# Kernel tuning notes

Measured on AMD Instinct MI355X. Metric: run time of the kernel, lower is better.

The kernel has to match this reference:

```python
import jax, jax.numpy as jnp
import numpy as np

DIM = 384

def setup_inputs() -> dict:
    key = jax.random.key(0)
    k1, k2, k3 = jax.random.split(key, 3)
    x = jax.random.normal(k1, (8, DIM, 56, 56), dtype=jnp.float32)
    # nn.Linear(dim, dim, bias=False): weight shape [out, in]; y = x @ W^T
    w1 = jax.random.normal(k2, (DIM, DIM), dtype=jnp.float32) * (1.0 / np.sqrt(DIM))
    w2 = jax.random.normal(k3, (DIM, DIM), dtype=jnp.float32) * (1.0 / np.sqrt(DIM))
    return {"x": x, "w1": w1, "w2": w2}

def reference(x, w1, w2):
    B, C, H, W = x.shape
    scale = C ** (-0.5)
    t = x.reshape(B, C, H * W).transpose(0, 2, 1)  # [B, N, C]
    q = jnp.einsum('bnc,dc->bnd', t, w1)           # linear1(x)
    attn = jnp.einsum('bnd,bmd->bnm', q, t) * scale  # QK^T scaled
    attn = jax.nn.softmax(attn, axis=-1)
    v = jnp.einsum('bnc,dc->bnd', t, w2)           # linear2(x)
    out = jnp.einsum('bnm,bmd->bnd', attn, v)      # [B, N, C]
    return out.transpose(0, 2, 1).reshape(B, C, H, W)
```

## Files before the change

### kernel.cpp

```cpp
#include <hip/hip_runtime.h>
#include <hip/hip_bf16.h>

#define DIM 384
#define SEQ 3136
#define NBATCH 8

typedef __attribute__((ext_vector_type(8))) short short8;
typedef __attribute__((ext_vector_type(4))) float fx4;
typedef __attribute__((ext_vector_type(4))) int i4;
typedef __hip_bfloat16 bf16;

#define MFMA(a,b,c) __builtin_amdgcn_mfma_f32_16x16x32_bf16(a,b,c,0,0,0)

__global__ __launch_bounds__(256) void ktrans(const float* __restrict__ x,
                                              bf16* __restrict__ kb) {
  __shared__ float t[64][65];
  int b = blockIdx.z;
  int n0 = blockIdx.x * 64, c0 = blockIdx.y * 64;
  int tid = threadIdx.x;
  {
    int nl = tid & 63, cl = tid >> 6;
    const float* xp = x + ((size_t)b * DIM + c0) * SEQ + n0;
    #pragma unroll
    for (int p = 0; p < 16; ++p) {
      int c = cl * 16 + p;
      t[c][nl] = xp[(size_t)c * SEQ + nl];
    }
  }
  __syncthreads();
  {
    int cc = tid & 63, nr = tid >> 6;
    bf16* kp = kb + ((size_t)b * SEQ + n0) * DIM + c0;
    #pragma unroll
    for (int p = 0; p < 16; ++p) {
      int n = nr * 16 + p;
      kp[(size_t)n * DIM + cc] = __float2bfloat16(t[cc][n]);
    }
  }
}

__global__ __launch_bounds__(256) void kwconv(const float* __restrict__ w1,
                                              const float* __restrict__ w2,
                                              bf16* __restrict__ w1b,
                                              bf16* __restrict__ w2b) {
  int i = blockIdx.x * 256 + threadIdx.x;
  w1b[i] = __float2bfloat16(w1[i]);
  w2b[i] = __float2bfloat16(w2[i]);
}

__global__ __launch_bounds__(256, 1) void kgemm(const bf16* __restrict__ A, long long Abs,
                                                const bf16* __restrict__ Bt, long long Bbs,
                                                bf16* __restrict__ out, long long Obs, int ldo) {
  __shared__ __align__(16) bf16 At[64][DIM + 8];
  __shared__ __align__(16) bf16 Bs[64][DIM + 8];
  int b = blockIdx.z;
  int tid = threadIdx.x;
  const bf16* Ab = A + (size_t)b * Abs + (size_t)blockIdx.x * 64 * DIM;
  const bf16* Bb = Bt + (size_t)b * Bbs + (size_t)blockIdx.y * 64 * DIM;
  {
    int row = tid >> 2, cb = (tid & 3) * 96;
    const i4* ga = (const i4*)(Ab + (size_t)row * DIM + cb);
    const i4* gb = (const i4*)(Bb + (size_t)row * DIM + cb);
    i4* la = (i4*)(&At[row][cb]);
    i4* lb = (i4*)(&Bs[row][cb]);
    #pragma unroll
    for (int p = 0; p < 12; ++p) { la[p] = ga[p]; lb[p] = gb[p]; }
  }
  __syncthreads();
  int wave = tid >> 6, lane = tid & 63;
  int r = lane & 15, kq = lane >> 4;
  fx4 zero = {0.f, 0.f, 0.f, 0.f};
  fx4 acc[4];
  #pragma unroll
  for (int i = 0; i < 4; ++i) acc[i] = zero;
  #pragma unroll
  for (int ks = 0; ks < 12; ++ks) {
    short8 af = *(const short8*)(&At[wave * 16 + r][ks * 32 + kq * 8]);
    #pragma unroll
    for (int ct = 0; ct < 4; ++ct) {
      short8 bfr = *(const short8*)(&Bs[ct * 16 + r][ks * 32 + kq * 8]);
      acc[ct] = MFMA(af, bfr, acc[ct]);
    }
  }
  bf16* ob = out + (size_t)b * Obs
           + (size_t)(blockIdx.x * 64 + wave * 16 + kq * 4) * ldo + blockIdx.y * 64;
  #pragma unroll
  for (int ct = 0; ct < 4; ++ct)
    #pragma unroll
    for (int rr = 0; rr < 4; ++rr)
      ob[(size_t)rr * ldo + ct * 16 + r] = __float2bfloat16(acc[ct][rr]);
}

__global__ __launch_bounds__(256, 2) void kattn(const bf16* __restrict__ Qb,
                                                const bf16* __restrict__ Kb,
                                                const bf16* __restrict__ Vt,
                                                float* __restrict__ out) {
  __shared__ __align__(16) bf16 Kl[64][DIM + 8];
  __shared__ __align__(16) bf16 Pl[4][16][68];
  __shared__ float rsum[64];

  int b = blockIdx.x;
  int n0 = blockIdx.y * 64;
  int tid = threadIdx.x;
  int wave = tid >> 6, lane = tid & 63;
  int r = lane & 15, kq = lane >> 4;

  short8 qf[12];
  {
    const bf16* qp = Qb + ((size_t)b * SEQ + n0 + wave * 16 + r) * DIM + kq * 8;
    #pragma unroll
    for (int ks = 0; ks < 12; ++ks) qf[ks] = *(const short8*)(qp + ks * 32);
  }
  fx4 zero = {0.f, 0.f, 0.f, 0.f};
  fx4 acc[4][6];
  #pragma unroll
  for (int i = 0; i < 4; ++i)
    #pragma unroll
    for (int j = 0; j < 6; ++j) acc[i][j] = zero;
  float rs[4] = {0.f, 0.f, 0.f, 0.f};
  const float cexp = 0.07362223f;

  const bf16* kbase = Kb + (size_t)b * SEQ * DIM;
  const bf16* vbase = Vt + (size_t)b * DIM * SEQ;

  int srow = tid >> 2, scb = (tid & 3) * 96;

  for (int im = 0; im < SEQ / 64; ++im) {
    int m0 = im * 64;
    {
      const i4* g = (const i4*)(kbase + (size_t)(m0 + srow) * DIM + scb);
      i4* l = (i4*)(&Kl[srow][scb]);
      #pragma unroll
      for (int p = 0; p < 12; ++p) l[p] = g[p];
    }
    short8 vf[2][6];
    #pragma unroll
    for (int ks2 = 0; ks2 < 2; ++ks2)
      #pragma unroll
      for (int dtl = 0; dtl < 6; ++dtl) {
        int d = (wave * 6 + dtl) * 16 + r;
        vf[ks2][dtl] = *(const short8*)(vbase + (size_t)d * SEQ + m0 + ks2 * 32 + kq * 8);
      }
    __syncthreads();
    fx4 sa[4];
    #pragma unroll
    for (int ct = 0; ct < 4; ++ct) sa[ct] = zero;
    #pragma unroll
    for (int ks = 0; ks < 12; ++ks) {
      #pragma unroll
      for (int ct = 0; ct < 4; ++ct) {
        short8 bfr = *(const short8*)(&Kl[ct * 16 + r][ks * 32 + kq * 8]);
        sa[ct] = MFMA(qf[ks], bfr, sa[ct]);
      }
    }
    #pragma unroll
    for (int rr = 0; rr < 4; ++rr) {
      float e0 = exp2f(sa[0][rr] * cexp);
      float e1 = exp2f(sa[1][rr] * cexp);
      float e2 = exp2f(sa[2][rr] * cexp);
      float e3 = exp2f(sa[3][rr] * cexp);
      int row = kq * 4 + rr;
      Pl[wave][row][r]      = __float2bfloat16(e0);
      Pl[wave][row][16 + r] = __float2bfloat16(e1);
      Pl[wave][row][32 + r] = __float2bfloat16(e2);
      Pl[wave][row][48 + r] = __float2bfloat16(e3);
      rs[rr] += (e0 + e1) + (e2 + e3);
    }
    __syncthreads();
    #pragma unroll
    for (int ks2 = 0; ks2 < 2; ++ks2) {
      short8 pa[4];
      #pragma unroll
      for (int rg = 0; rg < 4; ++rg)
        pa[rg] = *(const short8*)(&Pl[rg][r][ks2 * 32 + kq * 8]);
      #pragma unroll
      for (int dtl = 0; dtl < 6; ++dtl) {
        #pragma unroll
        for (int rg = 0; rg < 4; ++rg)
          acc[rg][dtl] = MFMA(pa[rg], vf[ks2][dtl], acc[rg][dtl]);
      }
    }
  }
  #pragma unroll
  for (int rr = 0; rr < 4; ++rr) {
    float v = rs[rr];
    v += __shfl_xor(v, 1);
    v += __shfl_xor(v, 2);
    v += __shfl_xor(v, 4);
    v += __shfl_xor(v, 8);
    if (r == 0) rsum[wave * 16 + kq * 4 + rr] = v;
  }
  __syncthreads();
  float* ob = out + (size_t)b * DIM * SEQ;
  #pragma unroll
  for (int rg = 0; rg < 4; ++rg) {
    #pragma unroll
    for (int rr = 0; rr < 4; ++rr) {
      float inv = 1.0f / rsum[rg * 16 + kq * 4 + rr];
      int n = n0 + rg * 16 + kq * 4 + rr;
      #pragma unroll
      for (int dtl = 0; dtl < 6; ++dtl) {
        int d = (wave * 6 + dtl) * 16 + r;
        ob[(size_t)d * SEQ + n] = acc[rg][dtl][rr] * inv;
      }
    }
  }
}

extern "C" void kernel_launch(void* const* d_in, const int* in_sizes, int n_in,
                              void* d_out, int out_size, void* d_ws, size_t ws_size,
                              hipStream_t stream) {
  const float* x  = (const float*)d_in[0];
  const float* w1 = (const float*)d_in[1];
  const float* w2 = (const float*)d_in[2];
  float* out = (float*)d_out;

  char* ws = (char*)d_ws;
  size_t SZ = (size_t)NBATCH * SEQ * DIM * sizeof(bf16);
  bf16* Kb  = (bf16*)(ws);
  bf16* Qb  = (bf16*)(ws + SZ);
  bf16* Vt  = (bf16*)(ws + 2 * SZ);
  bf16* w1b = (bf16*)(ws + 3 * SZ);
  bf16* w2b = (bf16*)(ws + 3 * SZ + (size_t)DIM * DIM * sizeof(bf16));

  ktrans<<<dim3(SEQ / 64, DIM / 64, NBATCH), 256, 0, stream>>>(x, Kb);
  kwconv<<<dim3(DIM * DIM / 256), 256, 0, stream>>>(w1, w2, w1b, w2b);
  kgemm<<<dim3(SEQ / 64, DIM / 64, NBATCH), 256, 0, stream>>>(
      Kb, (long long)SEQ * DIM, w1b, 0LL, Qb, (long long)SEQ * DIM, DIM);
  kgemm<<<dim3(DIM / 64, SEQ / 64, NBATCH), 256, 0, stream>>>(
      w2b, 0LL, Kb, (long long)SEQ * DIM, Vt, (long long)DIM * SEQ, SEQ);
  kattn<<<dim3(NBATCH, SEQ / 64), 256, 0, stream>>>(Qb, Kb, Vt, out);
}
```

Measured before the change: 305.7 us.

## Repartition attention kernel to 32-row query tiles with 8 waves per block

The attention kernel now processes 32 query rows per block with 512 threads. Waves split into 2 row groups times 4 key-column chunks for the QK^T stage, and each wave owns 48 output channels for the PV stage. Per-wave row sums are combined through shared memory. This doubles the block count and cuts per-thread accumulator registers, aiming for more occupancy and better latency hiding. In exchange, each K tile is loaded from global and LDS-staged twice as often per query row, which raises K/V traffic.

```diff
diff --git a/kernel.cpp b/kernel.cpp
--- a/kernel.cpp
+++ b/kernel.cpp
@@ -91,93 +91,83 @@
       ob[(size_t)rr * ldo + ct * 16 + r] = __float2bfloat16(acc[ct][rr]);
 }
 
-__global__ __launch_bounds__(256, 2) void kattn(const bf16* __restrict__ Qb,
+__global__ __launch_bounds__(512, 4) void kattn(const bf16* __restrict__ Qb,
                                                 const bf16* __restrict__ Kb,
                                                 const bf16* __restrict__ Vt,
                                                 float* __restrict__ out) {
   __shared__ __align__(16) bf16 Kl[64][DIM + 8];
-  __shared__ __align__(16) bf16 Pl[4][16][68];
-  __shared__ float rsum[64];
+  __shared__ __align__(16) bf16 Pl[2][16][68];
+  __shared__ float rsum2[4][32];
 
   int b = blockIdx.x;
-  int n0 = blockIdx.y * 64;
+  int n0 = blockIdx.y * 32;
   int tid = threadIdx.x;
   int wave = tid >> 6, lane = tid & 63;
   int r = lane & 15, kq = lane >> 4;
+  int rg = wave >> 2;
+  int ch = wave & 3;
 
   short8 qf[12];
   {
-    const bf16* qp = Qb + ((size_t)b * SEQ + n0 + wave * 16 + r) * DIM + kq * 8;
+    const bf16* qp = Qb + ((size_t)b * SEQ + n0 + rg * 16 + r) * DIM + kq * 8;
     #pragma unroll
     for (int ks = 0; ks < 12; ++ks) qf[ks] = *(const short8*)(qp + ks * 32);
   }
   fx4 zero = {0.f, 0.f, 0.f, 0.f};
-  fx4 acc[4][6];
-  #pragma unroll
-  for (int i = 0; i < 4; ++i)
-    #pragma unroll
-    for (int j = 0; j < 6; ++j) acc[i][j] = zero;
+  fx4 acc[2][3];
+  #pragma unroll
+  for (int i = 0; i < 2; ++i)
+    #pragma unroll
+    for (int j = 0; j < 3; ++j) acc[i][j] = zero;
   float rs[4] = {0.f, 0.f, 0.f, 0.f};
   const float cexp = 0.07362223f;
 
   const bf16* kbase = Kb + (size_t)b * SEQ * DIM;
   const bf16* vbase = Vt + (size_t)b * DIM * SEQ;
 
-  int srow = tid >> 2, scb = (tid & 3) * 96;
+  int krow = tid >> 3, kcs = (tid & 7) * 48;
 
   for (int im = 0; im < SEQ / 64; ++im) {
     int m0 = im * 64;
     {
-      const i4* g = (const i4*)(kbase + (size_t)(m0 + srow) * DIM + scb);
-      i4* l = (i4*)(&Kl[srow][scb]);
-      #pragma unroll
-      for (int p = 0; p < 12; ++p) l[p] = g[p];
-    }
-    short8 vf[2][6];
+      const i4* g = (const i4*)(kbase + (size_t)(m0 + krow) * DIM + kcs);
+      i4* l = (i4*)(&Kl[krow][kcs]);
+      #pragma unroll
+      for (int p = 0; p < 6; ++p) l[p] = g[p];
+    }
+    short8 vf[2][3];
     #pragma unroll
     for (int ks2 = 0; ks2 < 2; ++ks2)
       #pragma unroll
-      for (int dtl = 0; dtl < 6; ++dtl) {
-        int d = (wave * 6 + dtl) * 16 + r;
+      for (int dtl = 0; dtl < 3; ++dtl) {
+        int d = wave * 48 + dtl * 16 + r;
         vf[ks2][dtl] = *(const short8*)(vbase + (size_t)d * SEQ + m0 + ks2 * 32 + kq * 8);
       }
     __syncthreads();
-    fx4 sa[4];
-    #pragma unroll
-    for (int ct = 0; ct < 4; ++ct) sa[ct] = zero;
+    fx4 sa = zero;
     #pragma unroll
     for (int ks = 0; ks < 12; ++ks) {
-      #pragma unroll
-      for (int ct = 0; ct < 4; ++ct) {
-        short8 bfr = *(const short8*)(&Kl[ct * 16 + r][ks * 32 + kq * 8]);
-        sa[ct] = MFMA(qf[ks], bfr, sa[ct]);
-      }
+      short8 bfr = *(const short8*)(&Kl[ch * 16 + r][ks * 32 + kq * 8]);
+      sa = MFMA(qf[ks], bfr, sa);
     }
     #pragma unroll
     for (int rr = 0; rr < 4; ++rr) {
-      float e0 = exp2f(sa[0][rr] * cexp);
-      float e1 = exp2f(sa[1][rr] * cexp);
-      float e2 = exp2f(sa[2][rr] * cexp);
-      float e3 = exp2f(sa[3][rr] * cexp);
-      int row = kq * 4 + rr;
-      Pl[wave][row][r]      = __float2bfloat16(e0);
-      Pl[wave][row][16 + r] = __float2bfloat16(e1);
-      Pl[wave][row][32 + r] = __float2bfloat16(e2);
-      Pl[wave][row][48 + r] = __float2bfloat16(e3);
-      rs[rr] += (e0 + e1) + (e2 + e3);
+      float e0 = exp2f(sa[rr] * cexp);
+      Pl[rg][kq * 4 + rr][ch * 16 + r] = __float2bfloat16(e0);
+      rs[rr] += e0;
     }
     __syncthreads();
     #pragma unroll
     for (int ks2 = 0; ks2 < 2; ++ks2) {
-      short8 pa[4];
-      #pragma unroll
-      for (int rg = 0; rg < 4; ++rg)
-        pa[rg] = *(const short8*)(&Pl[rg][r][ks2 * 32 + kq * 8]);
-      #pragma unroll
-      for (int dtl = 0; dtl < 6; ++dtl) {
+      short8 pa[2];
+      #pragma unroll
+      for (int g2 = 0; g2 < 2; ++g2)
+        pa[g2] = *(const short8*)(&Pl[g2][r][ks2 * 32 + kq * 8]);
+      #pragma unroll
+      for (int dtl = 0; dtl < 3; ++dtl) {
         #pragma unroll
-        for (int rg = 0; rg < 4; ++rg)
-          acc[rg][dtl] = MFMA(pa[rg], vf[ks2][dtl], acc[rg][dtl]);
+        for (int g2 = 0; g2 < 2; ++g2)
+          acc[g2][dtl] = MFMA(pa[g2], vf[ks2][dtl], acc[g2][dtl]);
       }
     }
   }
@@ -188,20 +178,21 @@
     v += __shfl_xor(v, 2);
     v += __shfl_xor(v, 4);
     v += __shfl_xor(v, 8);
-    if (r == 0) rsum[wave * 16 + kq * 4 + rr] = v;
+    if (r == 0) rsum2[ch][rg * 16 + kq * 4 + rr] = v;
   }
   __syncthreads();
   float* ob = out + (size_t)b * DIM * SEQ;
   #pragma unroll
-  for (int rg = 0; rg < 4; ++rg) {
+  for (int g2 = 0; g2 < 2; ++g2) {
     #pragma unroll
     for (int rr = 0; rr < 4; ++rr) {
-      float inv = 1.0f / rsum[rg * 16 + kq * 4 + rr];
-      int n = n0 + rg * 16 + kq * 4 + rr;
-      #pragma unroll
-      for (int dtl = 0; dtl < 6; ++dtl) {
-        int d = (wave * 6 + dtl) * 16 + r;
-        ob[(size_t)d * SEQ + n] = acc[rg][dtl][rr] * inv;
+      int row = g2 * 16 + kq * 4 + rr;
+      float inv = 1.0f / (rsum2[0][row] + rsum2[1][row] + rsum2[2][row] + rsum2[3][row]);
+      int n = n0 + row;
+      #pragma unroll
+      for (int dtl = 0; dtl < 3; ++dtl) {
+        int d = wave * 48 + dtl * 16 + r;
+        ob[(size_t)d * SEQ + n] = acc[g2][dtl][rr] * inv;
       }
     }
   }
@@ -229,5 +220,5 @@
       Kb, (long long)SEQ * DIM, w1b, 0LL, Qb, (long long)SEQ * DIM, DIM);
   kgemm<<<dim3(DIM / 64, SEQ / 64, NBATCH), 256, 0, stream>>>(
       w2b, 0LL, Kb, (long long)SEQ * DIM, Vt, (long long)DIM * SEQ, SEQ);
-  kattn<<<dim3(NBATCH, SEQ / 64), 256, 0, stream>>>(Qb, Kb, Vt, out);
-}
+  kattn<<<dim3(NBATCH, SEQ / 32), 512, 0, stream>>>(Qb, Kb, Vt, out);
+}
```

Result: slower. 477.1 us (+56.1%).

## Use 2x2 wave tiling for QK^T to halve K fragment LDS reads

Applied to the files above, without the earlier changes.

In the attention kernel, the QK^T score computation now gives each wave a 32x32 tile (two Q row groups by two key column groups) instead of 16 rows by all 64 keys. Each K fragment read from LDS is therefore reused across two Q fragments, halving K LDS traffic per wave. The cost is doubling the Q fragments held in registers (24 short8) and keeping partial row sums per column half, which are combined at the end. The K tile staging copy is also split into two batches of six loads to limit live registers.

```diff
diff --git a/kernel.cpp b/kernel.cpp
--- a/kernel.cpp
+++ b/kernel.cpp
@@ -96,20 +96,23 @@
                                                 const bf16* __restrict__ Vt,
                                                 float* __restrict__ out) {
   __shared__ __align__(16) bf16 Kl[64][DIM + 8];
-  __shared__ __align__(16) bf16 Pl[4][16][68];
-  __shared__ float rsum[64];
+  __shared__ __align__(16) bf16 Pl[64][68];
+  __shared__ float rsum2[2][64];
 
   int b = blockIdx.x;
   int n0 = blockIdx.y * 64;
   int tid = threadIdx.x;
   int wave = tid >> 6, lane = tid & 63;
   int r = lane & 15, kq = lane >> 4;
-
-  short8 qf[12];
-  {
-    const bf16* qp = Qb + ((size_t)b * SEQ + n0 + wave * 16 + r) * DIM + kq * 8;
-    #pragma unroll
-    for (int ks = 0; ks < 12; ++ks) qf[ks] = *(const short8*)(qp + ks * 32);
+  int rh = wave >> 1;
+  int chh = wave & 1;
+
+  short8 qf[2][12];
+  #pragma unroll
+  for (int ri = 0; ri < 2; ++ri) {
+    const bf16* qp = Qb + ((size_t)b * SEQ + n0 + rh * 32 + ri * 16 + r) * DIM + kq * 8;
+    #pragma unroll
+    for (int ks = 0; ks < 12; ++ks) qf[ri][ks] = *(const short8*)(qp + ks * 32);
   }
   fx4 zero = {0.f, 0.f, 0.f, 0.f};
   fx4 acc[4][6];
@@ -117,7 +120,7 @@
   for (int i = 0; i < 4; ++i)
     #pragma unroll
     for (int j = 0; j < 6; ++j) acc[i][j] = zero;
-  float rs[4] = {0.f, 0.f, 0.f, 0.f};
+  float rs[2][4] = {{0.f, 0.f, 0.f, 0.f}, {0.f, 0.f, 0.f, 0.f}};
   const float cexp = 0.07362223f;
 
   const bf16* kbase = Kb + (size_t)b * SEQ * DIM;
@@ -130,8 +133,15 @@
     {
       const i4* g = (const i4*)(kbase + (size_t)(m0 + srow) * DIM + scb);
       i4* l = (i4*)(&Kl[srow][scb]);
-      #pragma unroll
-      for (int p = 0; p < 12; ++p) l[p] = g[p];
+      i4 t0[6];
+      #pragma unroll
+      for (int p = 0; p < 6; ++p) t0[p] = g[p];
+      #pragma unroll
+      for (int p = 0; p < 6; ++p) l[p] = t0[p];
+      #pragma unroll
+      for (int p = 0; p < 6; ++p) t0[p] = g[6 + p];
+      #pragma unroll
+      for (int p = 0; p < 6; ++p) l[6 + p] = t0[p];
     }
     short8 vf[2][6];
     #pragma unroll
@@ -142,37 +152,34 @@
         vf[ks2][dtl] = *(const short8*)(vbase + (size_t)d * SEQ + m0 + ks2 * 32 + kq * 8);
       }
     __syncthreads();
-    fx4 sa[4];
-    #pragma unroll
-    for (int ct = 0; ct < 4; ++ct) sa[ct] = zero;
+    fx4 sa[2][2] = {{zero, zero}, {zero, zero}};
     #pragma unroll
     for (int ks = 0; ks < 12; ++ks) {
-      #pragma unroll
-      for (int ct = 0; ct < 4; ++ct) {
-        short8 bfr = *(const short8*)(&Kl[ct * 16 + r][ks * 32 + kq * 8]);
-        sa[ct] = MFMA(qf[ks], bfr, sa[ct]);
-      }
-    }
-    #pragma unroll
-    for (int rr = 0; rr < 4; ++rr) {
-      float e0 = exp2f(sa[0][rr] * cexp);
-      float e1 = exp2f(sa[1][rr] * cexp);
-      float e2 = exp2f(sa[2][rr] * cexp);
-      float e3 = exp2f(sa[3][rr] * cexp);
-      int row = kq * 4 + rr;
-      Pl[wave][row][r]      = __float2bfloat16(e0);
-      Pl[wave][row][16 + r] = __float2bfloat16(e1);
-      Pl[wave][row][32 + r] = __float2bfloat16(e2);
-      Pl[wave][row][48 + r] = __float2bfloat16(e3);
-      rs[rr] += (e0 + e1) + (e2 + e3);
-    }
+      short8 b0 = *(const short8*)(&Kl[chh * 32 + r][ks * 32 + kq * 8]);
+      short8 b1 = *(const short8*)(&Kl[chh * 32 + 16 + r][ks * 32 + kq * 8]);
+      sa[0][0] = MFMA(qf[0][ks], b0, sa[0][0]);
+      sa[0][1] = MFMA(qf[0][ks], b1, sa[0][1]);
+      sa[1][0] = MFMA(qf[1][ks], b0, sa[1][0]);
+      sa[1][1] = MFMA(qf[1][ks], b1, sa[1][1]);
+    }
+    #pragma unroll
+    for (int ri = 0; ri < 2; ++ri)
+      #pragma unroll
+      for (int rr = 0; rr < 4; ++rr) {
+        float e0 = exp2f(sa[ri][0][rr] * cexp);
+        float e1 = exp2f(sa[ri][1][rr] * cexp);
+        int row = rh * 32 + ri * 16 + kq * 4 + rr;
+        Pl[row][chh * 32 + r]      = __float2bfloat16(e0);
+        Pl[row][chh * 32 + 16 + r] = __float2bfloat16(e1);
+        rs[ri][rr] += e0 + e1;
+      }
     __syncthreads();
     #pragma unroll
     for (int ks2 = 0; ks2 < 2; ++ks2) {
       short8 pa[4];
       #pragma unroll
       for (int rg = 0; rg < 4; ++rg)
-        pa[rg] = *(const short8*)(&Pl[rg][r][ks2 * 32 + kq * 8]);
+        pa[rg] = *(const short8*)(&Pl[rg * 16 + r][ks2 * 32 + kq * 8]);
       #pragma unroll
       for (int dtl = 0; dtl < 6; ++dtl) {
         #pragma unroll
@@ -182,22 +189,25 @@
     }
   }
   #pragma unroll
-  for (int rr = 0; rr < 4; ++rr) {
-    float v = rs[rr];
-    v += __shfl_xor(v, 1);
-    v += __shfl_xor(v, 2);
-    v += __shfl_xor(v, 4);
-    v += __shfl_xor(v, 8);
-    if (r == 0) rsum[wave * 16 + kq * 4 + rr] = v;
-  }
+  for (int ri = 0; ri < 2; ++ri)
+    #pragma unroll
+    for (int rr = 0; rr < 4; ++rr) {
+      float v = rs[ri][rr];
+      v += __shfl_xor(v, 1);
+      v += __shfl_xor(v, 2);
+      v += __shfl_xor(v, 4);
+      v += __shfl_xor(v, 8);
+      if (r == 0) rsum2[chh][rh * 32 + ri * 16 + kq * 4 + rr] = v;
+    }
   __syncthreads();
   float* ob = out + (size_t)b * DIM * SEQ;
   #pragma unroll
   for (int rg = 0; rg < 4; ++rg) {
     #pragma unroll
     for (int rr = 0; rr < 4; ++rr) {
-      float inv = 1.0f / rsum[rg * 16 + kq * 4 + rr];
-      int n = n0 + rg * 16 + kq * 4 + rr;
+      int row = rg * 16 + kq * 4 + rr;
+      float inv = 1.0f / (rsum2[0][row] + rsum2[1][row]);
+      int n = n0 + row;
       #pragma unroll
       for (int dtl = 0; dtl < 6; ++dtl) {
         int d = (wave * 6 + dtl) * 16 + r;
```

New measurement: 463.4 us. +51.6%, slower.

## Prefetch K tiles via direct global-to-LDS loads with XOR swizzle in attention

Applied to the files above, without the earlier changes.

Replaces the register-staged copy of each 64-row K tile into shared memory with asynchronous global_load_lds transfers. The next tile is issued right after the score phase, so its load overlaps the P·V MFMA work. The K layout drops the row padding and uses an XOR swizzle on 16-byte chunks so the MFMA fragment reads avoid bank conflicts. This adds an extra barrier per iteration and depends on the swizzled write addresses matching the read pattern exactly.

```diff
diff --git a/kernel.cpp b/kernel.cpp
--- a/kernel.cpp
+++ b/kernel.cpp
@@ -95,7 +95,7 @@
                                                 const bf16* __restrict__ Kb,
                                                 const bf16* __restrict__ Vt,
                                                 float* __restrict__ out) {
-  __shared__ __align__(16) bf16 Kl[64][DIM + 8];
+  __shared__ __align__(16) bf16 Kl[64][DIM];
   __shared__ __align__(16) bf16 Pl[4][16][68];
   __shared__ float rsum[64];
 
@@ -104,6 +104,7 @@
   int tid = threadIdx.x;
   int wave = tid >> 6, lane = tid & 63;
   int r = lane & 15, kq = lane >> 4;
+  int s7 = r & 7;
 
   short8 qf[12];
   {
@@ -122,17 +123,29 @@
 
   const bf16* kbase = Kb + (size_t)b * SEQ * DIM;
   const bf16* vbase = Vt + (size_t)b * DIM * SEQ;
-
-  int srow = tid >> 2, scb = (tid & 3) * 96;
+  const bf16* Klf = &Kl[0][0];
+
+#define STAGE_K(m0_)                                                            \
+  {                                                                             \
+    const bf16* ksrc = kbase + (size_t)(m0_) * DIM;                             \
+    _Pragma("unroll")                                                           \
+    for (int p = 0; p < 12; ++p) {                                              \
+      int q = p * 256 + tid;                                                    \
+      int row = q / 48;                                                         \
+      int cpos = q - row * 48;                                                  \
+      int ko = row * DIM + ((cpos ^ (row & 7)) << 3);                           \
+      __builtin_amdgcn_global_load_lds(                                         \
+          (const __attribute__((address_space(1))) unsigned int*)(ksrc + ko),   \
+          (__attribute__((address_space(3))) unsigned int*)((char*)Klf + ((p * 4 + wave) << 10)), \
+          16, 0, 0);                                                            \
+    }                                                                           \
+  }
+
+  STAGE_K(0);
+  __syncthreads();
 
   for (int im = 0; im < SEQ / 64; ++im) {
     int m0 = im * 64;
-    {
-      const i4* g = (const i4*)(kbase + (size_t)(m0 + srow) * DIM + scb);
-      i4* l = (i4*)(&Kl[srow][scb]);
-      #pragma unroll
-      for (int p = 0; p < 12; ++p) l[p] = g[p];
-    }
     short8 vf[2][6];
     #pragma unroll
     for (int ks2 = 0; ks2 < 2; ++ks2)
@@ -141,15 +154,15 @@
         int d = (wave * 6 + dtl) * 16 + r;
         vf[ks2][dtl] = *(const short8*)(vbase + (size_t)d * SEQ + m0 + ks2 * 32 + kq * 8);
       }
-    __syncthreads();
     fx4 sa[4];
     #pragma unroll
     for (int ct = 0; ct < 4; ++ct) sa[ct] = zero;
     #pragma unroll
     for (int ks = 0; ks < 12; ++ks) {
+      int sw = ((4 * ks + kq) ^ s7) << 3;
       #pragma unroll
       for (int ct = 0; ct < 4; ++ct) {
-        short8 bfr = *(const short8*)(&Kl[ct * 16 + r][ks * 32 + kq * 8]);
+        short8 bfr = *(const short8*)(Klf + (ct * 16 + r) * DIM + sw);
         sa[ct] = MFMA(qf[ks], bfr, sa[ct]);
       }
     }
@@ -167,6 +180,7 @@
       rs[rr] += (e0 + e1) + (e2 + e3);
     }
     __syncthreads();
+    if (im + 1 < SEQ / 64) STAGE_K(m0 + 64);
     #pragma unroll
     for (int ks2 = 0; ks2 < 2; ++ks2) {
       short8 pa[4];
@@ -180,6 +194,7 @@
           acc[rg][dtl] = MFMA(pa[rg], vf[ks2][dtl], acc[rg][dtl]);
       }
     }
+    __syncthreads();
   }
   #pragma unroll
   for (int rr = 0; rr < 4; ++rr) {
@@ -205,6 +220,7 @@
       }
     }
   }
+#undef STAGE_K
 }
 
 extern "C" void kernel_launch(void* const* d_in, const int* in_sizes, int n_in,
```

Result: slower. 385.2 us (+26.0%).
